# Kernel tuning notes

Hardware: AMD Instinct MI355X
Metric: run time of the kernel (lower is better)

## Reference

```python
import math
import jax, jax.numpy as jnp
import numpy as np

LN_2PI = math.log(2.0 * math.pi)


def _patches(x, K, s):
    # x: (N,1,h,w) -> (N,K*K,oh,ow); channel i*K+j is the (i,j)-shifted strided slice
    N, _, h, w = x.shape
    oh = (h - K) // s + 1
    ow = (w - K) // s + 1
    cols = [x[:, 0, i:i + s * (oh - 1) + 1:s, j:j + s * (ow - 1) + 1:s]
            for i in range(K) for j in range(K)]
    return jnp.stack(cols, axis=1)


def _em_routing(a, V, beta_a, beta_u, max_iter, C):
    # a: (b,ni,nj), V: (b,ni,nj,16)
    b, ni, nj, _ = V.shape
    ba = jnp.tile(beta_a, nj // C)[None, None, :]            # (1,1,nj)
    bu = jnp.tile(beta_u, nj // C)[None, None, :, None]      # (1,1,nj,1)
    R = jnp.full((b, ni, nj), 1.0 / nj, dtype=V.dtype)
    a_out = None
    miu = None
    for t in range(max_iter):
        lam = 0.01 * (1.0 - 0.95 ** (t + 1))
        R4 = (R * a)[..., None]                              # (b,ni,nj,1)
        coeff = jnp.maximum(R4.sum(1, keepdims=True), 1e-8)  # (b,1,nj,1)
        R4 = R4 / coeff
        miu = (R4 * V).sum(1, keepdims=True)                 # (b,1,nj,16)
        d2 = (V - miu) ** 2
        sigma = jnp.maximum((R4 * d2).sum(1, keepdims=True), 1e-8)
        log_sigma = jnp.log(sigma)
        cost = (bu + 0.5 * log_sigma) * coeff                # (b,1,nj,16)
        a_out = jax.nn.sigmoid(lam * (ba - cost.sum(-1)))    # (b,1,nj)
        if t != max_iter - 1:
            logp = -0.5 * (LN_2PI + log_sigma + d2 / sigma).sum(-1)  # (b,ni,nj)
            R = jax.nn.softmax(a_out * logp, axis=-1)
    return a_out[:, 0], miu[:, 0]


def _conv_capsule(a, M, W, beta_a, beta_u, B, C, K, stride, iters,
                  share=False, add_coord=False):
    bB, _, h, w = a.shape
    b = bB // B
    oh = (h - K) // stride + 1
    ow = (w - K) // stride + 1
    KK = K * K
    # pose patches -> (b,B,KK,1,oh*ow,4,4)
    Mp = _patches(M, K, stride).reshape(b, B, 4, 4, KK, 1, oh * ow)
    Mp = jnp.transpose(Mp, (0, 1, 4, 5, 6, 2, 3))
    if share:
        V = W[None, :, None, :, None] @ Mp                   # (b,B,KK,C,ohw,4,4)
    else:
        V = W[None, :, :, :, None] @ Mp
    if add_coord:
        ii = np.repeat(np.arange(K), K).astype(np.float32)
        jj = np.tile(np.arange(K), K).astype(np.float32)
        ll = np.repeat(np.arange(oh), ow).astype(np.float32)
        kk = np.tile(np.arange(ow), oh).astype(np.float32)
        pos_x = (stride * kk[None, :] + ii[:, None]) / w
        pos_y = (stride * ll[None, :] + jj[:, None]) / h
        coords = jnp.asarray(np.stack([pos_x, pos_y], -1))   # (KK,ohw,2)
        V = V.at[:, :, :, :, :, 0, :2].add(coords[None, None, :, None, :, :].astype(V.dtype))
    ap = _patches(a, K, stride).reshape(b, B * KK, oh * ow)
    a_i = jnp.tile(ap, (1, 1, C))                            # (b,B*KK,C*ohw)
    Vf = V.reshape(b, B * KK, C * oh * ow, 16)
    a_j, M_j = _em_routing(a_i, Vf, beta_a, beta_u, iters, C)
    a_out = a_j.reshape(b * C, 1, oh, ow)
    # faithful to original: permute(0,2,1) then flat view -> (b*C*16,1,oh,ow)
    M_out = jnp.transpose(M_j, (0, 2, 1)).reshape(b * C * 16, 1, oh, ow)
    return a_out, M_out


def setup_inputs() -> dict:
    key = jax.random.key(0)
    ks = jax.random.split(key, 16)
    f32 = jnp.float32
    eye = jnp.eye(4, dtype=f32)
    inp = {
        "x": jax.random.normal(ks[0], (16, 2, 32, 32), dtype=f32),
        "conv_w": 0.015 * jax.random.normal(ks[1], (32, 2, 5, 5), dtype=f32),
        "conv_b": jnp.zeros((32,), dtype=f32),
        "pose_w": 0.01 * jax.random.normal(ks[2], (512, 32), dtype=f32),
        "pose_b": jnp.zeros((512,), dtype=f32),
        "act_w": 0.01 * jax.random.normal(ks[3], (32, 32), dtype=f32),
        "act_b": jnp.zeros((32,), dtype=f32),
        "W2": eye[None, None] + jax.random.uniform(ks[4], (32, 9, 32, 4, 4), dtype=f32, minval=-0.03, maxval=0.03),
        "beta_a2": 0.1 * jax.random.normal(ks[5], (32,), dtype=f32),
        "beta_u2": 0.1 * jax.random.normal(ks[6], (32,), dtype=f32),
        "W3": eye[None, None] + jax.random.uniform(ks[7], (32, 9, 32, 4, 4), dtype=f32, minval=-0.03, maxval=0.03),
        "beta_a3": 0.1 * jax.random.normal(ks[8], (32,), dtype=f32),
        "beta_u3": 0.1 * jax.random.normal(ks[9], (32,), dtype=f32),
        "W4": eye[None] + jax.random.uniform(ks[10], (32, 5, 4, 4), dtype=f32, minval=-0.03, maxval=0.03),
        "beta_a4": 0.1 * jax.random.normal(ks[11], (5,), dtype=f32),
        "beta_u4": 0.1 * jax.random.normal(ks[12], (5,), dtype=f32),
    }
    return inp


def reference(x, conv_w, conv_b, pose_w, pose_b, act_w, act_b,
              W2, beta_a2, beta_u2, W3, beta_a3, beta_u3, W4, beta_a4, beta_u4):
    # stem conv 5x5 stride 2 + relu: (b,2,32,32) -> (b,32,14,14)
    fea = jax.lax.conv_general_dilated(
        x, conv_w, window_strides=(2, 2), padding="VALID",
        dimension_numbers=("NCHW", "OIHW", "NCHW")) + conv_b[None, :, None, None]
    fea = jax.nn.relu(fea)
    # primary capsules (1x1 convs)
    M = jnp.einsum("bchw,oc->bohw", fea, pose_w) + pose_b[None, :, None, None]
    a = jax.nn.sigmoid(jnp.einsum("bchw,oc->bohw", fea, act_w) + act_b[None, :, None, None])
    bsz, _, h, w = a.shape
    a = a.reshape(-1, 1, h, w)      # (b*32,1,14,14)
    M = M.reshape(-1, 1, h, w)      # (b*512,1,14,14)
    a, M = _conv_capsule(a, M, W2, beta_a2, beta_u2, B=32, C=32, K=3, stride=2, iters=3)
    a, M = _conv_capsule(a, M, W3, beta_a3, beta_u3, B=32, C=32, K=3, stride=1, iters=3)
    a, _ = _conv_capsule(a, M, W4, beta_a4, beta_u4, B=32, C=5, K=4, stride=1, iters=3,
                         share=True, add_coord=True)
    return a.reshape(x.shape[0], 5)
```

## Files before the change

kernel.cpp:

```cpp
#include <hip/hip_runtime.h>
#include <math.h>

#define LN2PI 1.83787706640934548356f

__global__ void k_stem(const float* __restrict__ x, const float* __restrict__ w,
                       const float* __restrict__ bias, float* __restrict__ fea) {
    int idx = blockIdx.x * blockDim.x + threadIdx.x;
    if (idx >= 16*32*14*14) return;
    int ox = idx % 14, oy = (idx/14) % 14, oc = (idx/196) % 32, b = idx/(196*32);
    float s = bias[oc];
    const float* xb = x + b*2*1024;
    const float* wc = w + oc*2*25;
    #pragma unroll
    for (int ic = 0; ic < 2; ++ic)
        #pragma unroll
        for (int ky = 0; ky < 5; ++ky)
            #pragma unroll
            for (int kx = 0; kx < 5; ++kx)
                s = fmaf(xb[ic*1024 + (oy*2+ky)*32 + (ox*2+kx)],
                         wc[ic*25 + ky*5 + kx], s);
    fea[idx] = fmaxf(s, 0.f);
}

__global__ void k_primary(const float* __restrict__ fea,
                          const float* __restrict__ pw, const float* __restrict__ pb,
                          const float* __restrict__ aw, const float* __restrict__ ab,
                          float* __restrict__ M, float* __restrict__ a) {
    int idx = blockIdx.x * blockDim.x + threadIdx.x;
    if (idx >= 16*544*196) return;
    int hw = idx % 196, o = (idx/196) % 544, b = idx/(196*544);
    const float* f = fea + b*32*196 + hw;
    if (o < 512) {
        float s = pb[o];
        #pragma unroll
        for (int c = 0; c < 32; ++c) s = fmaf(f[c*196], pw[o*32+c], s);
        M[(b*512+o)*196 + hw] = s;
    } else {
        int oo = o - 512;
        float s = ab[oo];
        #pragma unroll
        for (int c = 0; c < 32; ++c) s = fmaf(f[c*196], aw[oo*32+c], s);
        a[(b*32+oo)*196 + hw] = 1.f/(1.f + __expf(-s));
    }
}

__global__ void k_patch(const float* __restrict__ a_in, const float* __restrict__ M_in,
                        float* __restrict__ aP, float4* __restrict__ MpV,
                        int B, int K, int stride, int h, int w, int oh, int ow) {
    int P = oh*ow, KK = K*K, ni = B*KK;
    int idx = blockIdx.x * blockDim.x + threadIdx.x;
    if (idx >= 16*ni*P) return;
    int i = idx % ni, p = (idx/ni) % P, b = idx/(ni*P);
    int Bi = i / KK, kk = i % KK, ki = kk / K, kj = kk % K;
    int py = p / ow, px = p % ow;
    int src = (py*stride + ki)*w + (px*stride + kj);
    int hw = h*w;
    aP[idx] = a_in[(b*B + Bi)*hw + src];
    const float* Ms = M_in + (size_t)((b*B + Bi)*16)*hw + src;
    size_t base = (size_t)(b*P + p)*4;
    #pragma unroll
    for (int m4 = 0; m4 < 4; ++m4)
        MpV[(base + m4)*ni + i] = make_float4(Ms[(4*m4+0)*hw], Ms[(4*m4+1)*hw],
                                              Ms[(4*m4+2)*hw], Ms[(4*m4+3)*hw]);
}

__global__ void k_wt(const float* __restrict__ W, float4* __restrict__ WtV,
                     int NI, int C) {
    int idx = blockIdx.x * blockDim.x + threadIdx.x;
    if (idx >= NI*C) return;
    int i = idx % NI, c = idx/NI;
    const float* src = W + (size_t)(i*C + c)*16;
    #pragma unroll
    for (int m4 = 0; m4 < 4; ++m4)
        WtV[((size_t)c*4 + m4)*NI + i] = make_float4(src[4*m4+0], src[4*m4+1],
                                                     src[4*m4+2], src[4*m4+3]);
}

template<int NI, int NJ, int P, int C>
__global__ __launch_bounds__(256)
void k_stats(const float* __restrict__ aP, const float4* __restrict__ MpV,
             const float4* __restrict__ WtV, const float* __restrict__ svb,
             const float* __restrict__ mxs, const float* __restrict__ ism,
             const float* __restrict__ beta_a, const float* __restrict__ beta_u,
             float* __restrict__ statP,
             float* __restrict__ a_fin, float* __restrict__ M_fin,
             int t, float lam, int fin)
{
    constexpr int NIT = (NI + 63) / 64;
    constexpr int RS = 68;
    __shared__ float sRed[4][33*RS];
    int wave = threadIdx.x >> 6, lane = threadIdx.x & 63;
    int g  = blockIdx.x % (16*P);
    int cg = blockIdx.x / (16*P);
    int c  = cg*4 + wave;
    int bb = g / P, p = g % P;
    int j  = c*P + p;

    const float*  aPb = aP  + (size_t)(bb*P + p)*NI;
    const float4* Mb  = MpV + (size_t)(bb*P + p)*4*NI;
    const float4* Wb  = WtV + (size_t)c*4*NI;
    const float*  svr = svb + (size_t)(bb*NJ + j)*NI;
    const float*  mxb = mxs + bb*NI;
    const float*  imb = ism + bb*NI;

    float accw = 0.f, accm[16], acc2[16];
    #pragma unroll
    for (int m = 0; m < 16; ++m) { accm[m] = 0.f; acc2[m] = 0.f; }

    for (int it = 0; it < NIT; ++it) {
        int i = lane + it*64;
        if ((NI % 64 == 0) || (i < NI)) {
            float r;
            if (t == 0) r = 1.f / NJ;
            else        r = __expf(svr[i] - mxb[i]) * imb[i];
            float wgt = r * aPb[i];
            float4 m0 = Mb[0*NI + i], m1 = Mb[1*NI + i];
            float4 m2 = Mb[2*NI + i], m3 = Mb[3*NI + i];
            accw += wgt;
            #pragma unroll
            for (int rr = 0; rr < 4; ++rr) {
                float4 w = Wb[rr*NI + i];
                float v0 = fmaf(w.w, m3.x, fmaf(w.z, m2.x, fmaf(w.y, m1.x, w.x*m0.x)));
                float v1 = fmaf(w.w, m3.y, fmaf(w.z, m2.y, fmaf(w.y, m1.y, w.x*m0.y)));
                float v2 = fmaf(w.w, m3.z, fmaf(w.z, m2.z, fmaf(w.y, m1.z, w.x*m0.z)));
                float v3 = fmaf(w.w, m3.w, fmaf(w.z, m2.w, fmaf(w.y, m1.w, w.x*m0.w)));
                float t0 = wgt*v0, t1 = wgt*v1, t2 = wgt*v2, t3 = wgt*v3;
                accm[rr*4+0] += t0; acc2[rr*4+0] = fmaf(t0, v0, acc2[rr*4+0]);
                accm[rr*4+1] += t1; acc2[rr*4+1] = fmaf(t1, v1, acc2[rr*4+1]);
                accm[rr*4+2] += t2; acc2[rr*4+2] = fmaf(t2, v2, acc2[rr*4+2]);
                accm[rr*4+3] += t3; acc2[rr*4+3] = fmaf(t3, v3, acc2[rr*4+3]);
            }
        }
    }

    float* row = sRed[wave];
    row[0*RS + lane] = accw;
    #pragma unroll
    for (int m = 0; m < 16; ++m) {
        row[(1+m)*RS + lane]  = accm[m];
        row[(17+m)*RS + lane] = acc2[m];
    }
    float S = 0.f;
    if (lane < 33) {
        const float4* r4 = (const float4*)(row + lane*RS);
        float4 s4 = make_float4(0.f, 0.f, 0.f, 0.f);
        #pragma unroll
        for (int k = 0; k < 16; ++k) {
            float4 v = r4[k];
            s4.x += v.x; s4.y += v.y; s4.z += v.z; s4.w += v.w;
        }
        S = (s4.x + s4.y) + (s4.z + s4.w);
    }
    float coeff = fmaxf(__shfl(S, 0), 1e-8f);
    float Sn = S / coeff;
    bool sig_lane = (lane >= 17 && lane < 33);
    int src = sig_lane ? (lane - 16) : 0;
    float muk = __shfl(Sn, src);
    float lg = 0.f, iv = 0.f;
    if (sig_lane) {
        float s = fmaxf(Sn - muk*muk, 1e-8f);
        lg = __logf(s);
        iv = 1.f / s;
    }
    float v = sig_lane ? lg : 0.f;
    #pragma unroll
    for (int off = 1; off < 64; off <<= 1) v += __shfl_xor(v, off);
    float lsum = v;
    float ao = 1.f/(1.f + __expf(-(lam * (beta_a[j % C] - (16.f*beta_u[j % C] + 0.5f*lsum) * coeff))));
    float G = 0.f, H2 = 0.f, gmu2 = 0.f;
    if (sig_lane) {
        G = -0.5f*ao*iv;
        H2 = -2.f*G*muk;
        gmu2 = G*muk*muk;
    }
    float u = sig_lane ? gmu2 : 0.f;
    #pragma unroll
    for (int off = 1; off < 64; off <<= 1) u += __shfl_xor(u, off);
    float K1 = fmaf(-0.5f*ao, 16.f*LN2PI + lsum, u);

    float* st = statP + (size_t)(bb*NJ + j)*36;
    if (sig_lane) {
        st[lane-17]      = G;
        st[16 + lane-17] = H2;
    }
    if (lane == 0) st[32] = K1;
    if (fin) {
        if (lane == 0) a_fin[bb*NJ + j] = ao;
        if (lane >= 1 && lane < 17)
            M_fin[(size_t)(bb*16 + lane-1)*NJ + j] = Sn;
    }
}

template<int NI, int NJ, int P, int C>
__global__ __launch_bounds__(320)
void k_sv(const float4* __restrict__ MpV, const float4* __restrict__ WtV,
          const float* __restrict__ statP,
          float* __restrict__ svb, float* __restrict__ pmx, float* __restrict__ psm)
{
    int p = blockIdx.x % P, bb = blockIdx.x / P;
    int i = threadIdx.x;
    bool act = (i < NI);

    float4 m0, m1, m2, m3;
    if (act) {
        const float4* Mb = MpV + (size_t)(bb*P + p)*4*NI;
        m0 = Mb[0*NI+i]; m1 = Mb[1*NI+i]; m2 = Mb[2*NI+i]; m3 = Mb[3*NI+i];
    }
    float mx = -3.0e38f, sm = 0.f;

    for (int c = 0; c < C; ++c) {
        int j = c*P + p;
        const float* st = statP + (size_t)(bb*NJ + j)*36;
        if (act) {
            const float4* Wb = WtV + (size_t)c*4*NI;
            float4 w0 = Wb[0*NI+i], w1 = Wb[1*NI+i], w2 = Wb[2*NI+i], w3 = Wb[3*NI+i];
            float V[16];
            {
                float4 w = w0;
                V[0] = fmaf(w.w, m3.x, fmaf(w.z, m2.x, fmaf(w.y, m1.x, w.x*m0.x)));
                V[1] = fmaf(w.w, m3.y, fmaf(w.z, m2.y, fmaf(w.y, m1.y, w.x*m0.y)));
                V[2] = fmaf(w.w, m3.z, fmaf(w.z, m2.z, fmaf(w.y, m1.z, w.x*m0.z)));
                V[3] = fmaf(w.w, m3.w, fmaf(w.z, m2.w, fmaf(w.y, m1.w, w.x*m0.w)));
                w = w1;
                V[4] = fmaf(w.w, m3.x, fmaf(w.z, m2.x, fmaf(w.y, m1.x, w.x*m0.x)));
                V[5] = fmaf(w.w, m3.y, fmaf(w.z, m2.y, fmaf(w.y, m1.y, w.x*m0.y)));
                V[6] = fmaf(w.w, m3.z, fmaf(w.z, m2.z, fmaf(w.y, m1.z, w.x*m0.z)));
                V[7] = fmaf(w.w, m3.w, fmaf(w.z, m2.w, fmaf(w.y, m1.w, w.x*m0.w)));
                w = w2;
                V[8]  = fmaf(w.w, m3.x, fmaf(w.z, m2.x, fmaf(w.y, m1.x, w.x*m0.x)));
                V[9]  = fmaf(w.w, m3.y, fmaf(w.z, m2.y, fmaf(w.y, m1.y, w.x*m0.y)));
                V[10] = fmaf(w.w, m3.z, fmaf(w.z, m2.z, fmaf(w.y, m1.z, w.x*m0.z)));
                V[11] = fmaf(w.w, m3.w, fmaf(w.z, m2.w, fmaf(w.y, m1.w, w.x*m0.w)));
                w = w3;
                V[12] = fmaf(w.w, m3.x, fmaf(w.z, m2.x, fmaf(w.y, m1.x, w.x*m0.x)));
                V[13] = fmaf(w.w, m3.y, fmaf(w.z, m2.y, fmaf(w.y, m1.y, w.x*m0.y)));
                V[14] = fmaf(w.w, m3.z, fmaf(w.z, m2.z, fmaf(w.y, m1.z, w.x*m0.z)));
                V[15] = fmaf(w.w, m3.w, fmaf(w.z, m2.w, fmaf(w.y, m1.w, w.x*m0.w)));
            }
            float acc = 0.f;
            #pragma unroll
            for (int m = 0; m < 16; ++m) {
                float tmp = fmaf(V[m], st[m], st[16+m]);
                acc = fmaf(V[m], tmp, acc);
            }
            float sv = st[32] + acc;
            if (sv > mx) { sm = sm*__expf(mx - sv) + 1.f; mx = sv; }
            else         { sm += __expf(sv - mx); }
            svb[(size_t)(bb*NJ + j)*NI + i] = sv;
        }
    }
    if (act) {
        pmx[(size_t)p*(16*NI) + bb*NI + i] = mx;
        psm[(size_t)p*(16*NI) + bb*NI + i] = sm;
    }
}

__global__ void k_comb(const float* __restrict__ pmx, const float* __restrict__ psm,
                       float* __restrict__ mxs, float* __restrict__ ism,
                       int nch, int ntot)
{
    int idx = blockIdx.x * blockDim.x + threadIdx.x;
    if (idx >= ntot) return;
    float mx = -3.0e38f, sm = 0.f;
    for (int ch = 0; ch < nch; ++ch) {
        float m2 = pmx[(size_t)ch*ntot + idx];
        float s2 = psm[(size_t)ch*ntot + idx];
        float M = fmaxf(mx, m2);
        sm = sm*__expf(mx - M) + s2*__expf(m2 - M);
        mx = M;
    }
    mxs[idx] = mx;
    ism[idx] = 1.f / sm;
}

__global__ __launch_bounds__(512)
void k_layer4(const float* __restrict__ a3, const float* __restrict__ M3,
              const float* __restrict__ W4, const float* __restrict__ ba4,
              const float* __restrict__ bu4, float* __restrict__ out)
{
    __shared__ float sMt[16*512];
    __shared__ float sA[512];
    __shared__ float sW[2560];
    __shared__ float sR[2560];
    __shared__ float sStat[5][34];

    int b = blockIdx.x, tid = threadIdx.x;
    int lane = tid & 63, wave = tid >> 6;

    for (int k = tid; k < 8192; k += 512) {
        int i = k & 511, m = k >> 9;
        sMt[k] = M3[b*8192 + (i & ~15)*16 + m*16 + (i & 15)];
    }
    sA[tid] = a3[b*512 + tid];
    for (int k = tid; k < 2560; k += 512) { sW[k] = W4[k]; sR[k] = 0.2f; }
    __syncthreads();

    const float lams[3] = {5.0e-4f, 9.75e-4f, 1.426250e-3f};

    for (int t = 0; t < 3; ++t) {
        if (wave < 5) {
            int j = wave;
            float accw = 0.f, accm[16], acc2[16];
            #pragma unroll
            for (int m = 0; m < 16; ++m) { accm[m] = 0.f; acc2[m] = 0.f; }
            for (int u = 0; u < 8; ++u) {
                int i = u*64 + lane;
                float wgt = sR[i*5 + j] * sA[i];
                float Mm[16];
                #pragma unroll
                for (int m = 0; m < 16; ++m) Mm[m] = sMt[m*512 + i];
                const float* Wm = &sW[((i>>4)*5 + j)*16];
                float V[16];
                #pragma unroll
                for (int r = 0; r < 4; ++r)
                    #pragma unroll
                    for (int cc = 0; cc < 4; ++cc) {
                        float s = Wm[r*4+0]*Mm[0*4+cc];
                        s = fmaf(Wm[r*4+1], Mm[1*4+cc], s);
                        s = fmaf(Wm[r*4+2], Mm[2*4+cc], s);
                        s = fmaf(Wm[r*4+3], Mm[3*4+cc], s);
                        V[r*4+cc] = s;
                    }
                V[0] += (float)((i & 15) >> 2) * 0.25f;
                V[1] += (float)(i & 3) * 0.25f;
                accw += wgt;
                #pragma unroll
                for (int m = 0; m < 16; ++m) {
                    float t1 = wgt * V[m];
                    accm[m] += t1;
                    acc2[m] = fmaf(t1, V[m], acc2[m]);
                }
            }
            for (int off = 1; off < 64; off <<= 1) {
                accw += __shfl_xor(accw, off);
                #pragma unroll
                for (int m = 0; m < 16; ++m) accm[m] += __shfl_xor(accm[m], off);
                #pragma unroll
                for (int m = 0; m < 16; ++m) acc2[m] += __shfl_xor(acc2[m], off);
            }
            float coeff = fmaxf(accw, 1e-8f);
            float lsum = 0.f, mu[16], isv[16];
            #pragma unroll
            for (int m = 0; m < 16; ++m) {
                mu[m] = accm[m] / coeff;
                float s = fmaxf(acc2[m]/coeff - mu[m]*mu[m], 1e-8f);
                lsum += __logf(s);
                isv[m] = 1.f / s;
            }
            float ao = 1.f/(1.f + __expf(-(lams[t] * (ba4[j] - (16.f*bu4[j] + 0.5f*lsum) * coeff))));
            if (lane == 0) {
                #pragma unroll
                for (int m = 0; m < 16; ++m) { sStat[j][m] = mu[m]; sStat[j][16+m] = isv[m]; }
                sStat[j][32] = lsum; sStat[j][33] = ao;
            }
        }
        __syncthreads();
        if (t < 2) {
            int i = tid;
            float Mm[16];
            #pragma unroll
            for (int m = 0; m < 16; ++m) Mm[m] = sMt[m*512 + i];
            float sv[5], mxv = -3.0e38f;
            #pragma unroll
            for (int j = 0; j < 5; ++j) {
                const float* Wm = &sW[((i>>4)*5 + j)*16];
                float V[16];
                #pragma unroll
                for (int r = 0; r < 4; ++r)
                    #pragma unroll
                    for (int cc = 0; cc < 4; ++cc) {
                        float s = Wm[r*4+0]*Mm[0*4+cc];
                        s = fmaf(Wm[r*4+1], Mm[1*4+cc], s);
                        s = fmaf(Wm[r*4+2], Mm[2*4+cc], s);
                        s = fmaf(Wm[r*4+3], Mm[3*4+cc], s);
                        V[r*4+cc] = s;
                    }
                V[0] += (float)((i & 15) >> 2) * 0.25f;
                V[1] += (float)(i & 3) * 0.25f;
                float q = 0.f;
                #pragma unroll
                for (int m = 0; m < 16; ++m) {
                    float d = V[m] - sStat[j][m];
                    q = fmaf(d*d, sStat[j][16+m], q);
                }
                float logp = -0.5f * (16.f*LN2PI + sStat[j][32] + q);
                sv[j] = sStat[j][33] * logp;
                mxv = fmaxf(mxv, sv[j]);
            }
            float sum = 0.f;
            #pragma unroll
            for (int j = 0; j < 5; ++j) { sv[j] = __expf(sv[j] - mxv); sum += sv[j]; }
            float inv = 1.f / sum;
            #pragma unroll
            for (int j = 0; j < 5; ++j) sR[i*5 + j] = sv[j] * inv;
            __syncthreads();
        }
    }
    if (tid < 5) out[b*5 + tid] = sStat[tid][33];
}

template<int NI, int NJ, int P, int C>
static void run_em(hipStream_t stream,
                   const float* aP, const float4* MpV, const float4* WtV,
                   const float* ba, const float* bu,
                   float* statP, float* svb, float* mxs, float* ism,
                   float* pmx, float* psm,
                   float* a_fin, float* M_fin)
{
    const float lams[3] = {5.0e-4f, 9.75e-4f, 1.426250e-3f};
    for (int t = 0; t < 3; ++t) {
        k_stats<NI,NJ,P,C><<<16*NJ/4, 256, 0, stream>>>(
            aP, MpV, WtV, svb, mxs, ism, ba, bu, statP, a_fin, M_fin,
            t, lams[t], (t == 2) ? 1 : 0);
        if (t < 2) {
            k_sv<NI,NJ,P,C><<<16*P, 320, 0, stream>>>(MpV, WtV, statP, svb, pmx, psm);
            k_comb<<<(16*NI + 255)/256, 256, 0, stream>>>(pmx, psm, mxs, ism, P, 16*NI);
        }
    }
}

extern "C" void kernel_launch(void* const* d_in, const int* in_sizes, int n_in,
                              void* d_out, int out_size, void* d_ws, size_t ws_size,
                              hipStream_t stream) {
    (void)in_sizes; (void)n_in; (void)out_size; (void)ws_size;
    const float* x       = (const float*)d_in[0];
    const float* conv_w  = (const float*)d_in[1];
    const float* conv_b  = (const float*)d_in[2];
    const float* pose_w  = (const float*)d_in[3];
    const float* pose_b  = (const float*)d_in[4];
    const float* act_w   = (const float*)d_in[5];
    const float* act_b   = (const float*)d_in[6];
    const float* W2      = (const float*)d_in[7];
    const float* beta_a2 = (const float*)d_in[8];
    const float* beta_u2 = (const float*)d_in[9];
    const float* W3      = (const float*)d_in[10];
    const float* beta_a3 = (const float*)d_in[11];
    const float* beta_u3 = (const float*)d_in[12];
    const float* W4      = (const float*)d_in[13];
    const float* beta_a4 = (const float*)d_in[14];
    const float* beta_u4 = (const float*)d_in[15];

    float* ws    = (float*)d_ws;
    float* fea   = ws;
    float* a1    = fea   + 100352;
    float* M1    = a1    + 100352;
    float* aP    = M1    + 1605632;
    float* Mp    = aP    + 165888;
    float* Wt    = Mp    + 2654208;
    float* statP = Wt    + 147456;
    float* svb   = statP + 663552;
    float* mxs   = svb   + 5308416;
    float* ismb  = mxs   + 4608;
    float* pmx   = ismb  + 4608;
    float* psm   = pmx   + 165888;
    float* a2    = psm   + 165888;
    float* M2    = a2    + 18432;
    float* a3    = M2    + 294912;
    float* M3    = a3    + 8192;

    float4* MpV = (float4*)Mp;
    float4* WtV = (float4*)Wt;

    k_stem<<<(16*32*196 + 255)/256, 256, 0, stream>>>(x, conv_w, conv_b, fea);
    k_primary<<<(16*544*196 + 255)/256, 256, 0, stream>>>(fea, pose_w, pose_b,
                                                          act_w, act_b, M1, a1);

    k_patch<<<(16*288*36 + 255)/256, 256, 0, stream>>>(a1, M1, aP, MpV, 32, 3, 2, 14, 14, 6, 6);
    k_wt<<<(288*32 + 255)/256, 256, 0, stream>>>(W2, WtV, 288, 32);
    run_em<288,1152,36,32>(stream, aP, MpV, WtV, beta_a2, beta_u2,
                           statP, svb, mxs, ismb, pmx, psm, a2, M2);

    k_patch<<<(16*288*16 + 255)/256, 256, 0, stream>>>(a2, M2, aP, MpV, 32, 3, 1, 6, 6, 4, 4);
    k_wt<<<(288*32 + 255)/256, 256, 0, stream>>>(W3, WtV, 288, 32);
    run_em<288,512,16,32>(stream, aP, MpV, WtV, beta_a3, beta_u3,
                          statP, svb, mxs, ismb, pmx, psm, a3, M3);

    k_layer4<<<16, 512, 0, stream>>>(a3, M3, W4, beta_a4, beta_u4, (float*)d_out);
}
```

Measured before the change: 475.1 us.

## Compute two output capsules per wave in k_stats to reuse pose loads

Each wave in the EM statistics kernel now accumulates two output capsule types (c and c+C/2). The pose patches, activations and routing normalisers are loaded once and used for both, and the stats grid is halved. The cross-lane reduction now starts with xor-shuffles within groups of four lanes, which shrinks the shared-memory staging rows. A waves_per_eu hint lets the compiler use more registers for the doubled accumulator set, at the cost of lower occupancy. The pmx/psm workspace offsets are also enlarged.

```diff
diff --git a/kernel.cpp b/kernel.cpp
--- a/kernel.cpp
+++ b/kernel.cpp
@@ -77,7 +77,7 @@
 }
 
 template<int NI, int NJ, int P, int C>
-__global__ __launch_bounds__(256)
+__global__ __launch_bounds__(256) __attribute__((amdgpu_waves_per_eu(2,4)))
 void k_stats(const float* __restrict__ aP, const float4* __restrict__ MpV,
              const float4* __restrict__ WtV, const float* __restrict__ svb,
              const float* __restrict__ mxs, const float* __restrict__ ism,
@@ -87,107 +87,135 @@
              int t, float lam, int fin)
 {
     constexpr int NIT = (NI + 63) / 64;
-    constexpr int RS = 68;
+    constexpr int RS = 20;
     __shared__ float sRed[4][33*RS];
     int wave = threadIdx.x >> 6, lane = threadIdx.x & 63;
     int g  = blockIdx.x % (16*P);
     int cg = blockIdx.x / (16*P);
-    int c  = cg*4 + wave;
+    int c0 = cg*4 + wave;
+    int c1 = c0 + C/2;
     int bb = g / P, p = g % P;
-    int j  = c*P + p;
+    int j0 = c0*P + p, j1 = c1*P + p;
 
     const float*  aPb = aP  + (size_t)(bb*P + p)*NI;
     const float4* Mb  = MpV + (size_t)(bb*P + p)*4*NI;
-    const float4* Wb  = WtV + (size_t)c*4*NI;
-    const float*  svr = svb + (size_t)(bb*NJ + j)*NI;
+    const float4* Wb0 = WtV + (size_t)c0*4*NI;
+    const float4* Wb1 = WtV + (size_t)c1*4*NI;
+    const float*  sv0 = svb + (size_t)(bb*NJ + j0)*NI;
+    const float*  sv1 = svb + (size_t)(bb*NJ + j1)*NI;
     const float*  mxb = mxs + bb*NI;
     const float*  imb = ism + bb*NI;
 
-    float accw = 0.f, accm[16], acc2[16];
+    float aw[2], am[2][16], a2[2][16];
     #pragma unroll
-    for (int m = 0; m < 16; ++m) { accm[m] = 0.f; acc2[m] = 0.f; }
+    for (int s = 0; s < 2; ++s) {
+        aw[s] = 0.f;
+        #pragma unroll
+        for (int m = 0; m < 16; ++m) { am[s][m] = 0.f; a2[s][m] = 0.f; }
+    }
 
     for (int it = 0; it < NIT; ++it) {
         int i = lane + it*64;
         if ((NI % 64 == 0) || (i < NI)) {
-            float r;
-            if (t == 0) r = 1.f / NJ;
-            else        r = __expf(svr[i] - mxb[i]) * imb[i];
-            float wgt = r * aPb[i];
+            float apv = aPb[i];
+            float r0, r1;
+            if (t == 0) {
+                r0 = 1.f / NJ; r1 = 1.f / NJ;
+            } else {
+                float mxv = mxb[i], imv = imb[i];
+                r0 = __expf(sv0[i] - mxv) * imv;
+                r1 = __expf(sv1[i] - mxv) * imv;
+            }
+            float wg0 = r0 * apv, wg1 = r1 * apv;
             float4 m0 = Mb[0*NI + i], m1 = Mb[1*NI + i];
             float4 m2 = Mb[2*NI + i], m3 = Mb[3*NI + i];
-            accw += wgt;
-            #pragma unroll
-            for (int rr = 0; rr < 4; ++rr) {
-                float4 w = Wb[rr*NI + i];
-                float v0 = fmaf(w.w, m3.x, fmaf(w.z, m2.x, fmaf(w.y, m1.x, w.x*m0.x)));
-                float v1 = fmaf(w.w, m3.y, fmaf(w.z, m2.y, fmaf(w.y, m1.y, w.x*m0.y)));
-                float v2 = fmaf(w.w, m3.z, fmaf(w.z, m2.z, fmaf(w.y, m1.z, w.x*m0.z)));
-                float v3 = fmaf(w.w, m3.w, fmaf(w.z, m2.w, fmaf(w.y, m1.w, w.x*m0.w)));
-                float t0 = wgt*v0, t1 = wgt*v1, t2 = wgt*v2, t3 = wgt*v3;
-                accm[rr*4+0] += t0; acc2[rr*4+0] = fmaf(t0, v0, acc2[rr*4+0]);
-                accm[rr*4+1] += t1; acc2[rr*4+1] = fmaf(t1, v1, acc2[rr*4+1]);
-                accm[rr*4+2] += t2; acc2[rr*4+2] = fmaf(t2, v2, acc2[rr*4+2]);
-                accm[rr*4+3] += t3; acc2[rr*4+3] = fmaf(t3, v3, acc2[rr*4+3]);
+            aw[0] += wg0; aw[1] += wg1;
+            #pragma unroll
+            for (int s = 0; s < 2; ++s) {
+                const float4* Wb = (s == 0) ? Wb0 : Wb1;
+                float wg = (s == 0) ? wg0 : wg1;
+                #pragma unroll
+                for (int rr = 0; rr < 4; ++rr) {
+                    float4 w = Wb[rr*NI + i];
+                    float v0 = fmaf(w.w, m3.x, fmaf(w.z, m2.x, fmaf(w.y, m1.x, w.x*m0.x)));
+                    float v1 = fmaf(w.w, m3.y, fmaf(w.z, m2.y, fmaf(w.y, m1.y, w.x*m0.y)));
+                    float v2 = fmaf(w.w, m3.z, fmaf(w.z, m2.z, fmaf(w.y, m1.z, w.x*m0.z)));
+                    float v3 = fmaf(w.w, m3.w, fmaf(w.z, m2.w, fmaf(w.y, m1.w, w.x*m0.w)));
+                    float t0 = wg*v0, t1 = wg*v1, t2 = wg*v2, t3 = wg*v3;
+                    am[s][rr*4+0] += t0; a2[s][rr*4+0] = fmaf(t0, v0, a2[s][rr*4+0]);
+                    am[s][rr*4+1] += t1; a2[s][rr*4+1] = fmaf(t1, v1, a2[s][rr*4+1]);
+                    am[s][rr*4+2] += t2; a2[s][rr*4+2] = fmaf(t2, v2, a2[s][rr*4+2]);
+                    am[s][rr*4+3] += t3; a2[s][rr*4+3] = fmaf(t3, v3, a2[s][rr*4+3]);
+                }
             }
         }
     }
 
     float* row = sRed[wave];
-    row[0*RS + lane] = accw;
     #pragma unroll
-    for (int m = 0; m < 16; ++m) {
-        row[(1+m)*RS + lane]  = accm[m];
-        row[(17+m)*RS + lane] = acc2[m];
-    }
-    float S = 0.f;
-    if (lane < 33) {
-        const float4* r4 = (const float4*)(row + lane*RS);
-        float4 s4 = make_float4(0.f, 0.f, 0.f, 0.f);
-        #pragma unroll
-        for (int k = 0; k < 16; ++k) {
-            float4 v = r4[k];
-            s4.x += v.x; s4.y += v.y; s4.z += v.z; s4.w += v.w;
-        }
-        S = (s4.x + s4.y) + (s4.z + s4.w);
-    }
-    float coeff = fmaxf(__shfl(S, 0), 1e-8f);
-    float Sn = S / coeff;
-    bool sig_lane = (lane >= 17 && lane < 33);
-    int src = sig_lane ? (lane - 16) : 0;
-    float muk = __shfl(Sn, src);
-    float lg = 0.f, iv = 0.f;
-    if (sig_lane) {
-        float s = fmaxf(Sn - muk*muk, 1e-8f);
-        lg = __logf(s);
-        iv = 1.f / s;
-    }
-    float v = sig_lane ? lg : 0.f;
-    #pragma unroll
-    for (int off = 1; off < 64; off <<= 1) v += __shfl_xor(v, off);
-    float lsum = v;
-    float ao = 1.f/(1.f + __expf(-(lam * (beta_a[j % C] - (16.f*beta_u[j % C] + 0.5f*lsum) * coeff))));
-    float G = 0.f, H2 = 0.f, gmu2 = 0.f;
-    if (sig_lane) {
-        G = -0.5f*ao*iv;
-        H2 = -2.f*G*muk;
-        gmu2 = G*muk*muk;
-    }
-    float u = sig_lane ? gmu2 : 0.f;
-    #pragma unroll
-    for (int off = 1; off < 64; off <<= 1) u += __shfl_xor(u, off);
-    float K1 = fmaf(-0.5f*ao, 16.f*LN2PI + lsum, u);
-
-    float* st = statP + (size_t)(bb*NJ + j)*36;
-    if (sig_lane) {
-        st[lane-17]      = G;
-        st[16 + lane-17] = H2;
-    }
-    if (lane == 0) st[32] = K1;
-    if (fin) {
-        if (lane == 0) a_fin[bb*NJ + j] = ao;
-        if (lane >= 1 && lane < 17)
-            M_fin[(size_t)(bb*16 + lane-1)*NJ + j] = Sn;
+    for (int s = 0; s < 2; ++s) {
+        int j = (s == 0) ? j0 : j1;
+        float accw = aw[s];
+        accw += __shfl_xor(accw, 1); accw += __shfl_xor(accw, 2);
+        #pragma unroll
+        for (int m = 0; m < 16; ++m) {
+            am[s][m] += __shfl_xor(am[s][m], 1); am[s][m] += __shfl_xor(am[s][m], 2);
+            a2[s][m] += __shfl_xor(a2[s][m], 1); a2[s][m] += __shfl_xor(a2[s][m], 2);
+        }
+        if ((lane & 3) == 0) {
+            int grp = lane >> 2;
+            row[0*RS + grp] = accw;
+            #pragma unroll
+            for (int m = 0; m < 16; ++m) {
+                row[(1+m)*RS + grp]  = am[s][m];
+                row[(17+m)*RS + grp] = a2[s][m];
+            }
+        }
+        float S = 0.f;
+        if (lane < 33) {
+            const float4* r4 = (const float4*)(row + lane*RS);
+            float4 a = r4[0], b4 = r4[1], c4 = r4[2], d4 = r4[3];
+            S = (((a.x+a.y)+(a.z+a.w)) + ((b4.x+b4.y)+(b4.z+b4.w)))
+              + (((c4.x+c4.y)+(c4.z+c4.w)) + ((d4.x+d4.y)+(d4.z+d4.w)));
+        }
+        float coeff = fmaxf(__shfl(S, 0), 1e-8f);
+        float Sn = S / coeff;
+        bool sig_lane = (lane >= 17 && lane < 33);
+        int src = sig_lane ? (lane - 16) : 0;
+        float muk = __shfl(Sn, src);
+        float lg = 0.f, iv = 0.f;
+        if (sig_lane) {
+            float sg = fmaxf(Sn - muk*muk, 1e-8f);
+            lg = __logf(sg);
+            iv = 1.f / sg;
+        }
+        float v = sig_lane ? lg : 0.f;
+        #pragma unroll
+        for (int off = 1; off < 64; off <<= 1) v += __shfl_xor(v, off);
+        float lsum = v;
+        float ao = 1.f/(1.f + __expf(-(lam * (beta_a[j % C] - (16.f*beta_u[j % C] + 0.5f*lsum) * coeff))));
+        float G = 0.f, H2 = 0.f, gmu2 = 0.f;
+        if (sig_lane) {
+            G = -0.5f*ao*iv;
+            H2 = -2.f*G*muk;
+            gmu2 = G*muk*muk;
+        }
+        float u = sig_lane ? gmu2 : 0.f;
+        #pragma unroll
+        for (int off = 1; off < 64; off <<= 1) u += __shfl_xor(u, off);
+        float K1 = fmaf(-0.5f*ao, 16.f*LN2PI + lsum, u);
+
+        float* st = statP + (size_t)(bb*NJ + j)*36;
+        if (sig_lane) {
+            st[lane-17]      = G;
+            st[16 + lane-17] = H2;
+        }
+        if (lane == 0) st[32] = K1;
+        if (fin) {
+            if (lane == 0) a_fin[bb*NJ + j] = ao;
+            if (lane >= 1 && lane < 17)
+                M_fin[(size_t)(bb*16 + lane-1)*NJ + j] = Sn;
+        }
     }
 }
 
@@ -409,7 +437,7 @@
 {
     const float lams[3] = {5.0e-4f, 9.75e-4f, 1.426250e-3f};
     for (int t = 0; t < 3; ++t) {
-        k_stats<NI,NJ,P,C><<<16*NJ/4, 256, 0, stream>>>(
+        k_stats<NI,NJ,P,C><<<16*NJ/8, 256, 0, stream>>>(
             aP, MpV, WtV, svb, mxs, ism, ba, bu, statP, a_fin, M_fin,
             t, lams[t], (t == 2) ? 1 : 0);
         if (t < 2) {
@@ -452,8 +480,8 @@
     float* mxs   = svb   + 5308416;
     float* ismb  = mxs   + 4608;
     float* pmx   = ismb  + 4608;
-    float* psm   = pmx   + 165888;
-    float* a2    = psm   + 165888;
+    float* psm   = pmx   + 331776;
+    float* a2    = psm   + 331776;
     float* M2    = a2    + 18432;
     float* a3    = M2    + 294912;
     float* M3    = a3    + 8192;
```

Measured after the change: 504.9 us. +6.3%, slower.
